# Optimization experiments

Measured on AMD Instinct MI355X. Metric: run time of the kernel, lower is better.

The kernel has to match this reference:

```python
import jax, jax.numpy as jnp
import numpy as np

H = 16  # num heads

def setup_inputs() -> dict:
    key = jax.random.key(0)
    k1, k2, k3 = jax.random.split(key, 3)
    B, L, D = 2, 2048, 1024
    x = jax.random.normal(k1, (B, L, D), dtype=jnp.float32)
    # torch Linear weight is [out,in]; we store transposed [in,out] so y = x @ W
    w_qkv = jax.random.normal(k2, (D, 3 * D), dtype=jnp.float32) * (D ** -0.5)
    w_proj = jax.random.normal(k3, (D, D), dtype=jnp.float32) * (D ** -0.5)
    return {"x": x, "w_qkv": w_qkv, "w_proj": w_proj, "num_prefix_tokens": 256}

def _prefix_causal_mask(L: int, M: int):
    # True = masked. Strict upper triangle (causal), then text rows (M:) may
    # see ALL prefix columns (:M).
    mask = jnp.triu(jnp.ones((L, L), dtype=bool), k=1)
    mask = mask.at[M:, :M].set(False)
    return mask

def reference(x, w_qkv, w_proj, num_prefix_tokens):
    B, L, D = x.shape
    d = D // H
    scale = d ** -0.5
    qkv = (x @ w_qkv).reshape(B, L, 3, H, d)
    q = jnp.transpose(qkv[:, :, 0], (0, 2, 1, 3))  # [B,H,L,d]
    k = jnp.transpose(qkv[:, :, 1], (0, 2, 1, 3))
    v = jnp.transpose(qkv[:, :, 2], (0, 2, 1, 3))
    logits = jnp.einsum("bhqd,bhkd->bhqk", q, k) * scale  # [B,H,L,L]
    mask = _prefix_causal_mask(L, num_prefix_tokens)
    logits = jnp.where(mask[None, None], -jnp.inf, logits)
    attn = jax.nn.softmax(logits, axis=-1)
    out = jnp.einsum("bhqk,bhkd->bhqd", attn, v)  # [B,H,L,d]
    out = jnp.transpose(out, (0, 2, 1, 3)).reshape(B, L, D)
    return out @ w_proj
```

## Files before the change

### kernel.cpp

```cpp
#include <hip/hip_runtime.h>
#include <hip/hip_bf16.h>

#define BATCH   2
#define L_SEQ   2048
#define DMODEL  1024
#define NHEADS  16
#define DHEAD   64
#define SEG     (BATCH*NHEADS*L_SEQ*DHEAD)

typedef __attribute__((ext_vector_type(8)))  short bf16x8;
typedef __attribute__((ext_vector_type(4)))  float f32x4;
typedef __attribute__((ext_vector_type(16))) float f32x16;

__device__ __forceinline__ unsigned short f2b(float f) {
    unsigned int u = __float_as_uint(f);
    return (unsigned short)((u + 0x7FFFu + ((u >> 16) & 1u)) >> 16);
}
__device__ __forceinline__ unsigned int pk2(float a, float b) {
    __hip_bfloat162 h = __float22bfloat162_rn(make_float2(a, b));
    return *(unsigned int*)&h;
}
__device__ __forceinline__ void glds16(const unsigned short* g, unsigned short* l) {
    __builtin_amdgcn_global_load_lds(
        (const __attribute__((address_space(1))) unsigned int*)g,
        (__attribute__((address_space(3))) unsigned int*)l, 16, 0, 0);
}

__device__ __forceinline__ void tcast64(const float* __restrict__ in,
                                        unsigned short* __restrict__ out,
                                        int K, int N, int bx, int by, int t) {
    __shared__ unsigned short T[64][65];
    const int k0 = by * 64, n0 = bx * 64;
    const int r = t >> 4, c4 = (t & 15) * 4;
#pragma unroll
    for (int rep = 0; rep < 4; ++rep) {
        int kk = rep * 16 + r;
        float4 f = *(const float4*)&in[(size_t)(k0 + kk) * N + n0 + c4];
        T[kk][c4 + 0] = f2b(f.x);
        T[kk][c4 + 1] = f2b(f.y);
        T[kk][c4 + 2] = f2b(f.z);
        T[kk][c4 + 3] = f2b(f.w);
    }
    __syncthreads();
#pragma unroll
    for (int rep = 0; rep < 4; ++rep) {
        int nn = rep * 16 + r;
        ushort4 o;
        o.x = T[c4 + 0][nn];
        o.y = T[c4 + 1][nn];
        o.z = T[c4 + 2][nn];
        o.w = T[c4 + 3][nn];
        *(ushort4*)&out[(size_t)(n0 + nn) * K + k0 + c4] = o;
    }
}

__global__ __launch_bounds__(256)
void prep(const float* __restrict__ x, const float* __restrict__ wqkv,
          const float* __restrict__ wproj, unsigned short* __restrict__ xb,
          unsigned short* __restrict__ wqkvT, unsigned short* __restrict__ wprojT) {
    const int id = blockIdx.x, t = threadIdx.x;
    if (id < 4096) {
        int i = id * 1024 + t * 4;
        float4 f = *(const float4*)&x[i];
        ushort4 o;
        o.x = f2b(f.x); o.y = f2b(f.y); o.z = f2b(f.z); o.w = f2b(f.w);
        *(ushort4*)&xb[i] = o;
    } else if (id < 4864) {
        int lid = id - 4096;
        tcast64(wqkv, wqkvT, DMODEL, 3 * DMODEL, lid % 48, lid / 48, t);
    } else {
        int lid = id - 4864;
        tcast64(wproj, wprojT, DMODEL, DMODEL, lid & 15, lid >> 4, t);
    }
}

__global__ __launch_bounds__(256)
void gemm_qkv(const unsigned short* __restrict__ A, const unsigned short* __restrict__ Bt,
              unsigned short* __restrict__ Cb) {
    __shared__ unsigned short SLDS[2 * 128 * 128];

    const int t = threadIdx.x;
    const int lane = t & 63, wave = t >> 6;
    const int quad = lane >> 4, l16 = lane & 15;
    const int wm = (wave >> 1) * 64, wn = (wave & 1) * 64;
    const int id = blockIdx.y * gridDim.x + blockIdx.x;
    const int xcd = id & 7, sq = id >> 3;
    const int m0 = (xcd * 4 + sq / 24) * 128;
    const int n0 = (sq % 24) * 128;
    const bool vrole = (n0 >= 2048);

    const int gsw = (lane & 7) ^ (lane >> 3);
    const unsigned short* ga[4];
    const unsigned short* gb[4];
    int ldA[4], ldB[4];
#pragma unroll
    for (int i = 0; i < 4; ++i) {
        int row = wave * 32 + i * 8 + (lane >> 3);
        ga[i] = &A[(size_t)(m0 + row) * DMODEL + gsw * 8];
        gb[i] = &Bt[(size_t)(n0 + row) * DMODEL + gsw * 8];
        ldA[i] = (wave * 32 + i * 8) * 64;
        ldB[i] = 8192 + (wave * 32 + i * 8) * 64;
    }
    const int sx = l16 & 7;

    f32x4 acc[4][4];
#pragma unroll
    for (int i = 0; i < 4; ++i)
#pragma unroll
        for (int j = 0; j < 4; ++j)
#pragma unroll
            for (int r = 0; r < 4; ++r) acc[i][j][r] = 0.0f;

#pragma unroll
    for (int i = 0; i < 4; ++i) {
        glds16(ga[i], &SLDS[ldA[i]]);
        glds16(gb[i], &SLDS[ldB[i]]);
    }
    __syncthreads();

    int cur = 0;
    for (int kt = 0; kt < 16; ++kt) {
        if (kt < 15) {
            const int ko = (kt + 1) * 64;
            unsigned short* dst = &SLDS[(cur ^ 1) * 16384];
#pragma unroll
            for (int i = 0; i < 4; ++i) {
                glds16(ga[i] + ko, dst + ldA[i]);
                glds16(gb[i] + ko, dst + ldB[i]);
            }
        }
        const unsigned short* Asm = &SLDS[cur * 16384];
        const unsigned short* Bsm = Asm + 8192;
#pragma unroll
        for (int s = 0; s < 2; ++s) {
            bf16x8 af[4], bfr[4];
#pragma unroll
            for (int i = 0; i < 4; ++i)
                af[i] = *(const bf16x8*)&Asm[(wm + i * 16 + l16) * 64 + ((4 * s + quad) ^ sx) * 8];
#pragma unroll
            for (int j = 0; j < 4; ++j)
                bfr[j] = *(const bf16x8*)&Bsm[(wn + j * 16 + l16) * 64 + ((4 * s + quad) ^ sx) * 8];
            __builtin_amdgcn_s_setprio(1);
            if (!vrole) {
#pragma unroll
                for (int i = 0; i < 4; ++i)
#pragma unroll
                    for (int j = 0; j < 4; ++j)
                        acc[i][j] = __builtin_amdgcn_mfma_f32_16x16x32_bf16(af[i], bfr[j], acc[i][j], 0, 0, 0);
            } else {
#pragma unroll
                for (int i = 0; i < 4; ++i)
#pragma unroll
                    for (int j = 0; j < 4; ++j)
                        acc[i][j] = __builtin_amdgcn_mfma_f32_16x16x32_bf16(bfr[j], af[i], acc[i][j], 0, 0, 0);
            }
            __builtin_amdgcn_s_setprio(0);
        }
        __syncthreads();
        cur ^= 1;
    }

    const float qscale = 0.1803368801111244f;
    const float scl = (!vrole && n0 < 1024) ? qscale : 1.0f;
#pragma unroll
    for (int i = 0; i < 4; ++i)
#pragma unroll
        for (int r = 0; r < 4; ++r) {
#pragma unroll
            for (int j = 0; j < 4; ++j) {
                int row_l, col_l;
                if (!vrole) {
                    row_l = wm + i * 16 + quad * 4 + r;
                    col_l = wn + j * 16 + l16;
                } else {
                    row_l = wn + j * 16 + quad * 4 + r;
                    col_l = wm + i * 16 + l16;
                }
                int key = row_l & 7;
                SLDS[row_l * 128 + (((col_l >> 3) ^ key) * 8) + (col_l & 7)] =
                    f2b(acc[i][j][r] * scl);
            }
        }
    __syncthreads();

    const int s0 = n0 >> 10;
    const int bb = m0 >> 11;
#pragma unroll
    for (int it = 0; it < 4; ++it) {
        int row = it * 32 + (t >> 3);
        int c = t & 7;
        int key = row & 7;
        bf16x8 v0 = *(const bf16x8*)&SLDS[row * 128 + ((c ^ key) * 8)];
        bf16x8 v1 = *(const bf16x8*)&SLDS[row * 128 + (((c + 8) ^ key) * 8)];
        if (!vrole) {
            int token = m0 + row, lp = token & (L_SEQ - 1);
            int n_a = n0 + c * 8,        h_a = (n_a >> 6) & 15, d_a = n_a & 63;
            int n_b = n0 + (c + 8) * 8,  h_b = (n_b >> 6) & 15, d_b = n_b & 63;
            size_t base = (size_t)s0 * SEG;
            *(bf16x8*)&Cb[base + (((size_t)(bb * NHEADS + h_a) * L_SEQ + lp) * DHEAD) + d_a] = v0;
            *(bf16x8*)&Cb[base + (((size_t)(bb * NHEADS + h_b) * L_SEQ + lp) * DHEAD) + d_b] = v1;
        } else {
            int fr = (n0 - 2048) + row;
            int h = fr >> 6, dd = fr & 63;
            int lp0 = (m0 & (L_SEQ - 1));
            size_t base = 2 * (size_t)SEG +
                          (((size_t)(bb * NHEADS + h) * DHEAD + dd) * L_SEQ) + lp0;
            *(bf16x8*)&Cb[base + c * 8]       = v0;
            *(bf16x8*)&Cb[base + (c + 8) * 8] = v1;
        }
    }
}

__global__ __launch_bounds__(256)
void gemm_proj(const unsigned short* __restrict__ A, const unsigned short* __restrict__ Bt,
               float* __restrict__ Cf) {
    __shared__ unsigned short SLDS[2 * 128 * 128];

    const int t = threadIdx.x;
    const int lane = t & 63, wave = t >> 6;
    const int quad = lane >> 4, l16 = lane & 15;
    const int wm = (wave >> 1) * 64, wn = (wave & 1) * 64;
    const int id = blockIdx.y * gridDim.x + blockIdx.x;
    const int xcd = id & 7, sq = id >> 3;
    const int m0 = (xcd * 4 + (sq >> 3)) * 128;
    const int n0 = (sq & 7) * 128;

    const int gsw = (lane & 7) ^ (lane >> 3);
    const unsigned short* ga[4];
    const unsigned short* gb[4];
    int ldA[4], ldB[4];
#pragma unroll
    for (int i = 0; i < 4; ++i) {
        int row = wave * 32 + i * 8 + (lane >> 3);
        ga[i] = &A[(size_t)(m0 + row) * DMODEL + gsw * 8];
        gb[i] = &Bt[(size_t)(n0 + row) * DMODEL + gsw * 8];
        ldA[i] = (wave * 32 + i * 8) * 64;
        ldB[i] = 8192 + (wave * 32 + i * 8) * 64;
    }
    const int sx = l16 & 7;

    f32x4 acc[4][4];
#pragma unroll
    for (int i = 0; i < 4; ++i)
#pragma unroll
        for (int j = 0; j < 4; ++j)
#pragma unroll
            for (int r = 0; r < 4; ++r) acc[i][j][r] = 0.0f;

#pragma unroll
    for (int i = 0; i < 4; ++i) {
        glds16(ga[i], &SLDS[ldA[i]]);
        glds16(gb[i], &SLDS[ldB[i]]);
    }
    __syncthreads();

    int cur = 0;
    for (int kt = 0; kt < 16; ++kt) {
        if (kt < 15) {
            const int ko = (kt + 1) * 64;
            unsigned short* dst = &SLDS[(cur ^ 1) * 16384];
#pragma unroll
            for (int i = 0; i < 4; ++i) {
                glds16(ga[i] + ko, dst + ldA[i]);
                glds16(gb[i] + ko, dst + ldB[i]);
            }
        }
        const unsigned short* Asm = &SLDS[cur * 16384];
        const unsigned short* Bsm = Asm + 8192;
#pragma unroll
        for (int s = 0; s < 2; ++s) {
            bf16x8 af[4], bfr[4];
#pragma unroll
            for (int i = 0; i < 4; ++i)
                af[i] = *(const bf16x8*)&Asm[(wm + i * 16 + l16) * 64 + ((4 * s + quad) ^ sx) * 8];
#pragma unroll
            for (int j = 0; j < 4; ++j)
                bfr[j] = *(const bf16x8*)&Bsm[(wn + j * 16 + l16) * 64 + ((4 * s + quad) ^ sx) * 8];
            __builtin_amdgcn_s_setprio(1);
#pragma unroll
            for (int i = 0; i < 4; ++i)
#pragma unroll
                for (int j = 0; j < 4; ++j)
                    acc[i][j] = __builtin_amdgcn_mfma_f32_16x16x32_bf16(af[i], bfr[j], acc[i][j], 0, 0, 0);
            __builtin_amdgcn_s_setprio(0);
        }
        __syncthreads();
        cur ^= 1;
    }

#pragma unroll
    for (int i = 0; i < 4; ++i)
#pragma unroll
        for (int r = 0; r < 4; ++r) {
            int row = m0 + wm + i * 16 + quad * 4 + r;
#pragma unroll
            for (int j = 0; j < 4; ++j)
                Cf[(size_t)row * DMODEL + n0 + wn + j * 16 + l16] = acc[i][j][r];
        }
}

__global__ __launch_bounds__(512)
void attn_mfma(const unsigned short* __restrict__ Qg, const unsigned short* __restrict__ Kg,
               const unsigned short* __restrict__ Vg, unsigned short* __restrict__ Ao) {
    __shared__ unsigned short SLDS[24576];
    __shared__ float Rex[192];
    unsigned short* Ksm = SLDS;
    unsigned short* Vsm = SLDS + 8192;
    unsigned short* Psm = SLDS + 16384;

    const int t = threadIdx.x;
    const int lane = t & 63, wave = t >> 6;
    const int l31 = lane & 31, hi = lane >> 5;
    const int bh = blockIdx.x & 31;
    const int Qt = 31 - (blockIdx.x >> 5);
    const int q0 = Qt * 64;
    const int qh = wave & 1, kp = wave >> 1;
    const int wq0 = q0 + qh * 32;
    const int nstrip = (Qt >> 1) + 1;
    const int b = bh >> 4, h = bh & 15;
    const size_t qkbase = (size_t)bh * L_SEQ * DHEAD;
    const size_t vbase  = (size_t)bh * DHEAD * L_SEQ;

    bf16x8 bq[4];
#pragma unroll
    for (int ks = 0; ks < 4; ++ks)
        bq[ks] = *(const bf16x8*)&Qg[qkbase + (size_t)(wq0 + l31) * DHEAD + ks * 16 + hi * 8];

    const int kc0 = t & 7,  kr0 = (t >> 3) * 2;
    const int vc0 = t & 15, vd0 = (t >> 4) * 2;

    unsigned short* Pw = Psm + wave * 1024;

    f32x16 O0, O1;
#pragma unroll
    for (int r = 0; r < 16; ++r) { O0[r] = 0.0f; O1[r] = 0.0f; }
    float rs = 0.0f;

    bf16x8 gk[2], gv[2];
#pragma unroll
    for (int i = 0; i < 2; ++i) {
        gk[i] = *(const bf16x8*)&Kg[qkbase + (size_t)(kr0 + i) * DHEAD + kc0 * 8];
        gv[i] = *(const bf16x8*)&Vg[vbase + (size_t)(vd0 + i) * L_SEQ + vc0 * 8];
    }

    for (int s = 0; s < nstrip; ++s) {
        __syncthreads();
#pragma unroll
        for (int i = 0; i < 2; ++i) {
            *(bf16x8*)&Ksm[(kc0 * 128 + ((kr0 + i) ^ kc0)) * 8] = gk[i];
            *(bf16x8*)&Vsm[(vc0 * 64 + ((vd0 + i) ^ vc0)) * 8] = gv[i];
        }
        if (s + 1 < nstrip) {
            const int kn = (s + 1) * 128;
#pragma unroll
            for (int i = 0; i < 2; ++i) {
                gk[i] = *(const bf16x8*)&Kg[qkbase + (size_t)(kn + kr0 + i) * DHEAD + kc0 * 8];
                gv[i] = *(const bf16x8*)&Vg[vbase + (size_t)(vd0 + i) * L_SEQ + kn + vc0 * 8];
            }
        }
        __syncthreads();

        const int keybase = s * 128 + kp * 32;
        if (keybase <= wq0 + 31) {
            f32x16 ST;
#pragma unroll
            for (int r = 0; r < 16; ++r) ST[r] = 0.0f;
            __builtin_amdgcn_s_setprio(1);
#pragma unroll
            for (int ks = 0; ks < 4; ++ks) {
                const int c = ks * 2 + hi;
                const int rk = kp * 32 + l31;
                bf16x8 a = *(const bf16x8*)&Ksm[(c * 128 + (rk ^ c)) * 8];
                ST = __builtin_amdgcn_mfma_f32_32x32x16_bf16(a, bq[ks], ST, 0, 0, 0);
            }
            __builtin_amdgcn_s_setprio(0);

            if (keybase + 31 > wq0) {
                const int qg = wq0 + l31;
#pragma unroll
                for (int r = 0; r < 16; ++r) {
                    int keyg = keybase + (r & 3) + 8 * (r >> 2) + 4 * hi;
                    if (keyg > qg) ST[r] = -1e30f;
                }
            }

#pragma unroll
            for (int g = 0; g < 4; ++g) {
                float p0 = __builtin_amdgcn_exp2f(ST[4 * g + 0]);
                float p1 = __builtin_amdgcn_exp2f(ST[4 * g + 1]);
                float p2 = __builtin_amdgcn_exp2f(ST[4 * g + 2]);
                float p3 = __builtin_amdgcn_exp2f(ST[4 * g + 3]);
                rs += (p0 + p1) + (p2 + p3);
                *(uint2*)&Pw[(g * 32 + (l31 ^ g)) * 8 + hi * 4] =
                    make_uint2(pk2(p0, p1), pk2(p2, p3));
            }

            __builtin_amdgcn_s_setprio(1);
#pragma unroll
            for (int ks = 0; ks < 2; ++ks) {
                const int cp = ks * 2 + hi;
                const int cv = kp * 4 + cp;
                bf16x8 pa = *(const bf16x8*)&Pw[(cp * 32 + (l31 ^ cp)) * 8];
                bf16x8 v0 = *(const bf16x8*)&Vsm[(cv * 64 + (l31 ^ cv)) * 8];
                bf16x8 v1 = *(const bf16x8*)&Vsm[(cv * 64 + ((32 + l31) ^ cv)) * 8];
                O0 = __builtin_amdgcn_mfma_f32_32x32x16_bf16(pa, v0, O0, 0, 0, 0);
                O1 = __builtin_amdgcn_mfma_f32_32x32x16_bf16(pa, v1, O1, 0, 0, 0);
            }
            __builtin_amdgcn_s_setprio(0);
        }
    }

    rs += __shfl_xor(rs, 32, 64);

    __syncthreads();
    float* Oex = (float*)SLDS;
    if (kp != 0) {
        const int g = (qh * 3 + (kp - 1)) * 2048;
#pragma unroll
        for (int r = 0; r < 16; ++r) {
            int qloc = (r & 3) + 8 * (r >> 2) + 4 * hi;
            Oex[g + qloc * 64 + l31]      = O0[r];
            Oex[g + qloc * 64 + 32 + l31] = O1[r];
        }
        if (hi == 0) Rex[(qh * 3 + (kp - 1)) * 32 + l31] = rs;
    }
    __syncthreads();
    if (kp == 0) {
        float rs_tot = rs;
#pragma unroll
        for (int p = 0; p < 3; ++p) rs_tot += Rex[(qh * 3 + p) * 32 + l31];
        float linv = 1.0f / rs_tot;
        float lf[16];
#pragma unroll
        for (int r = 0; r < 16; ++r) {
            int qloc = (r & 3) + 8 * (r >> 2) + 4 * hi;
#pragma unroll
            for (int p = 0; p < 3; ++p) {
                O0[r] += Oex[(qh * 3 + p) * 2048 + qloc * 64 + l31];
                O1[r] += Oex[(qh * 3 + p) * 2048 + qloc * 64 + 32 + l31];
            }
            lf[r] = __shfl(linv, qloc, 32);
        }
#pragma unroll
        for (int r = 0; r < 16; ++r) {
            int qloc = (r & 3) + 8 * (r >> 2) + 4 * hi;
            int token = wq0 + qloc;
            size_t ob = ((size_t)(b * L_SEQ + token)) * DMODEL + h * DHEAD;
            Ao[ob + l31]      = f2b(O0[r] * lf[r]);
            Ao[ob + 32 + l31] = f2b(O1[r] * lf[r]);
        }
    }
}

extern "C" void kernel_launch(void* const* d_in, const int* in_sizes, int n_in,
                              void* d_out, int out_size, void* d_ws, size_t ws_size,
                              hipStream_t stream) {
    const float* x      = (const float*)d_in[0];
    const float* w_qkv  = (const float*)d_in[1];
    const float* w_proj = (const float*)d_in[2];
    float* out = (float*)d_out;

    unsigned short* ws     = (unsigned short*)d_ws;
    unsigned short* xb     = ws;
    unsigned short* wqkvT  = xb + 4194304;
    unsigned short* wprojT = wqkvT + 3145728;
    unsigned short* qkv    = wprojT + 1048576;
    unsigned short* ao     = qkv + 3 * (size_t)SEG;

    prep<<<5120, 256, 0, stream>>>(x, w_qkv, w_proj, xb, wqkvT, wprojT);

    gemm_qkv<<<dim3(24, 32), 256, 0, stream>>>(xb, wqkvT, qkv);

    attn_mfma<<<1024, 512, 0, stream>>>(qkv, qkv + SEG, qkv + 2 * (size_t)SEG, ao);

    gemm_proj<<<dim3(8, 32), 256, 0, stream>>>(ao, wprojT, out);
}
```

Baseline: 170.0 us.

## Keep softmax probabilities in registers via lane shuffles instead of LDS round-trip

The P tile produced by the QK^T MFMA is now repacked into the PV MFMA operand layout with cross-half-wave shuffles, instead of being written to LDS and read back. This drops the per-wave P scratch area and shrinks shared memory from 48KB to 32KB. To fit the smaller buffer, the final cross-wave output reduction becomes a two-stage tree with extra barriers. The risks are added shuffle/select instructions and more synchronisation in the epilogue.

```diff
diff --git a/kernel.cpp b/kernel.cpp
--- a/kernel.cpp
+++ b/kernel.cpp
@@ -11,6 +11,7 @@
 typedef __attribute__((ext_vector_type(8)))  short bf16x8;
 typedef __attribute__((ext_vector_type(4)))  float f32x4;
 typedef __attribute__((ext_vector_type(16))) float f32x16;
+typedef __attribute__((ext_vector_type(4)))  unsigned int u32x4;
 
 __device__ __forceinline__ unsigned short f2b(float f) {
     unsigned int u = __float_as_uint(f);
@@ -302,11 +303,10 @@
 __global__ __launch_bounds__(512)
 void attn_mfma(const unsigned short* __restrict__ Qg, const unsigned short* __restrict__ Kg,
                const unsigned short* __restrict__ Vg, unsigned short* __restrict__ Ao) {
-    __shared__ unsigned short SLDS[24576];
+    __shared__ unsigned short SLDS[16384];
     __shared__ float Rex[192];
     unsigned short* Ksm = SLDS;
     unsigned short* Vsm = SLDS + 8192;
-    unsigned short* Psm = SLDS + 16384;
 
     const int t = threadIdx.x;
     const int lane = t & 63, wave = t >> 6;
@@ -329,8 +329,6 @@
     const int kc0 = t & 7,  kr0 = (t >> 3) * 2;
     const int vc0 = t & 15, vd0 = (t >> 4) * 2;
 
-    unsigned short* Pw = Psm + wave * 1024;
-
     f32x16 O0, O1;
 #pragma unroll
     for (int r = 0; r < 16; ++r) { O0[r] = 0.0f; O1[r] = 0.0f; }
@@ -384,27 +382,45 @@
                 }
             }
 
-#pragma unroll
-            for (int g = 0; g < 4; ++g) {
-                float p0 = __builtin_amdgcn_exp2f(ST[4 * g + 0]);
-                float p1 = __builtin_amdgcn_exp2f(ST[4 * g + 1]);
-                float p2 = __builtin_amdgcn_exp2f(ST[4 * g + 2]);
-                float p3 = __builtin_amdgcn_exp2f(ST[4 * g + 3]);
-                rs += (p0 + p1) + (p2 + p3);
-                *(uint2*)&Pw[(g * 32 + (l31 ^ g)) * 8 + hi * 4] =
-                    make_uint2(pk2(p0, p1), pk2(p2, p3));
-            }
+            float p[16];
+#pragma unroll
+            for (int r = 0; r < 16; ++r) p[r] = __builtin_amdgcn_exp2f(ST[r]);
+#pragma unroll
+            for (int g = 0; g < 4; ++g)
+                rs += ((p[4*g] + p[4*g+1]) + (p[4*g+2] + p[4*g+3]));
+
+            unsigned int wv0 = pk2(p[0],  p[1]),  wv1 = pk2(p[2],  p[3]);
+            unsigned int wv2 = pk2(p[4],  p[5]),  wv3 = pk2(p[6],  p[7]);
+            unsigned int wv4 = pk2(p[8],  p[9]),  wv5 = pk2(p[10], p[11]);
+            unsigned int wv6 = pk2(p[12], p[13]), wv7 = pk2(p[14], p[15]);
+            unsigned int xv0 = (unsigned)__shfl_xor((int)wv0, 32, 64);
+            unsigned int xv1 = (unsigned)__shfl_xor((int)wv1, 32, 64);
+            unsigned int xv2 = (unsigned)__shfl_xor((int)wv2, 32, 64);
+            unsigned int xv3 = (unsigned)__shfl_xor((int)wv3, 32, 64);
+            unsigned int xv4 = (unsigned)__shfl_xor((int)wv4, 32, 64);
+            unsigned int xv5 = (unsigned)__shfl_xor((int)wv5, 32, 64);
+            unsigned int xv6 = (unsigned)__shfl_xor((int)wv6, 32, 64);
+            unsigned int xv7 = (unsigned)__shfl_xor((int)wv7, 32, 64);
+            u32x4 d0, d1;
+            d0[0] = hi ? xv2 : wv0;  d0[1] = hi ? xv3 : wv1;
+            d0[2] = hi ? wv2 : xv0;  d0[3] = hi ? wv3 : xv1;
+            d1[0] = hi ? xv6 : wv4;  d1[1] = hi ? xv7 : wv5;
+            d1[2] = hi ? wv6 : xv4;  d1[3] = hi ? wv7 : xv5;
+            bf16x8 pa0 = __builtin_bit_cast(bf16x8, d0);
+            bf16x8 pa1 = __builtin_bit_cast(bf16x8, d1);
 
             __builtin_amdgcn_s_setprio(1);
-#pragma unroll
-            for (int ks = 0; ks < 2; ++ks) {
-                const int cp = ks * 2 + hi;
-                const int cv = kp * 4 + cp;
-                bf16x8 pa = *(const bf16x8*)&Pw[(cp * 32 + (l31 ^ cp)) * 8];
-                bf16x8 v0 = *(const bf16x8*)&Vsm[(cv * 64 + (l31 ^ cv)) * 8];
-                bf16x8 v1 = *(const bf16x8*)&Vsm[(cv * 64 + ((32 + l31) ^ cv)) * 8];
-                O0 = __builtin_amdgcn_mfma_f32_32x32x16_bf16(pa, v0, O0, 0, 0, 0);
-                O1 = __builtin_amdgcn_mfma_f32_32x32x16_bf16(pa, v1, O1, 0, 0, 0);
+            {
+                const int cv0 = kp * 4 + hi;
+                bf16x8 v0 = *(const bf16x8*)&Vsm[(cv0 * 64 + (l31 ^ cv0)) * 8];
+                bf16x8 v1 = *(const bf16x8*)&Vsm[(cv0 * 64 + ((32 + l31) ^ cv0)) * 8];
+                O0 = __builtin_amdgcn_mfma_f32_32x32x16_bf16(pa0, v0, O0, 0, 0, 0);
+                O1 = __builtin_amdgcn_mfma_f32_32x32x16_bf16(pa0, v1, O1, 0, 0, 0);
+                const int cv1 = kp * 4 + 2 + hi;
+                bf16x8 v2 = *(const bf16x8*)&Vsm[(cv1 * 64 + (l31 ^ cv1)) * 8];
+                bf16x8 v3 = *(const bf16x8*)&Vsm[(cv1 * 64 + ((32 + l31) ^ cv1)) * 8];
+                O0 = __builtin_amdgcn_mfma_f32_32x32x16_bf16(pa1, v2, O0, 0, 0, 0);
+                O1 = __builtin_amdgcn_mfma_f32_32x32x16_bf16(pa1, v3, O1, 0, 0, 0);
             }
             __builtin_amdgcn_s_setprio(0);
         }
@@ -414,15 +430,35 @@
 
     __syncthreads();
     float* Oex = (float*)SLDS;
-    if (kp != 0) {
-        const int g = (qh * 3 + (kp - 1)) * 2048;
+    if (kp >= 2) {
+        const int g = (qh * 2 + (kp - 2)) * 2048;
 #pragma unroll
         for (int r = 0; r < 16; ++r) {
             int qloc = (r & 3) + 8 * (r >> 2) + 4 * hi;
             Oex[g + qloc * 64 + l31]      = O0[r];
             Oex[g + qloc * 64 + 32 + l31] = O1[r];
         }
-        if (hi == 0) Rex[(qh * 3 + (kp - 1)) * 32 + l31] = rs;
+    }
+    if (kp != 0 && hi == 0) Rex[(qh * 3 + (kp - 1)) * 32 + l31] = rs;
+    __syncthreads();
+    if (kp < 2) {
+        const int g = (qh * 2 + kp) * 2048;
+#pragma unroll
+        for (int r = 0; r < 16; ++r) {
+            int qloc = (r & 3) + 8 * (r >> 2) + 4 * hi;
+            O0[r] += Oex[g + qloc * 64 + l31];
+            O1[r] += Oex[g + qloc * 64 + 32 + l31];
+        }
+    }
+    __syncthreads();
+    if (kp == 1) {
+        const int g = qh * 2048;
+#pragma unroll
+        for (int r = 0; r < 16; ++r) {
+            int qloc = (r & 3) + 8 * (r >> 2) + 4 * hi;
+            Oex[g + qloc * 64 + l31]      = O0[r];
+            Oex[g + qloc * 64 + 32 + l31] = O1[r];
+        }
     }
     __syncthreads();
     if (kp == 0) {
@@ -434,11 +470,8 @@
 #pragma unroll
         for (int r = 0; r < 16; ++r) {
             int qloc = (r & 3) + 8 * (r >> 2) + 4 * hi;
-#pragma unroll
-            for (int p = 0; p < 3; ++p) {
-                O0[r] += Oex[(qh * 3 + p) * 2048 + qloc * 64 + l31];
-                O1[r] += Oex[(qh * 3 + p) * 2048 + qloc * 64 + 32 + l31];
-            }
+            O0[r] += Oex[qh * 2048 + qloc * 64 + l31];
+            O1[r] += Oex[qh * 2048 + qloc * 64 + 32 + l31];
             lf[r] = __shfl(linv, qloc, 32);
         }
 #pragma unroll
```

Result: slower. 174.5 us (+2.7%).
